# Optimization experiments

Measured on AMD Instinct MI355X. Metric: run time of the kernel, lower is better.

## Reference

```python
import jax, jax.numpy as jnp
import numpy as np


def silu(x):
    return x * jax.nn.sigmoid(x)


def setup_inputs() -> dict:
    key = jax.random.key(0)
    B, L, Din = 2, 512, 128
    E, K = 2, 4
    d = E * Din          # inner dim = 256
    N = d                # state size forced to hid_dim = expansion*input_dim
    R = d // 16          # dt low-rank = 16
    ks = jax.random.split(key, 12)
    s = 0.02
    rn = lambda k, sh: (jax.random.normal(k, sh, jnp.float32) * s)
    return {
        "x":      jax.random.normal(ks[0], (B, L, Din), jnp.float32),
        "W_in":   rn(ks[1], (Din, d)),  "b_in":  jnp.zeros((d,), jnp.float32),
        "W_res":  rn(ks[2], (Din, d)),  "b_res": jnp.zeros((d,), jnp.float32),
        "conv_w": rn(ks[3], (d, d, K)), "conv_b": jnp.zeros((d,), jnp.float32),
        "W_xdt":  rn(ks[4], (d, R)),
        "W_dt":   rn(ks[5], (R, d)),
        "b_dt":   jnp.full((d,), -4.6, jnp.float32),  # softplus -> dt ~ 0.01
        "W_B":    rn(ks[6], (d, N)),
        "W_C":    rn(ks[7], (d, N)),
        "A_log":  jnp.log(jnp.broadcast_to(jnp.arange(1, N + 1, dtype=jnp.float32), (d, N))),
        "D":      jnp.ones((d,), jnp.float32),
        "W_out":  rn(ks[8], (d, Din)), "b_out": jnp.zeros((Din,), jnp.float32),
    }


def reference(x, W_in, b_in, W_res, b_res, conv_w, conv_b,
              W_xdt, W_dt, b_dt, W_B, W_C, A_log, D, W_out, b_out):
    k = conv_w.shape[-1]
    # input projections
    xi = x @ W_in + b_in               # [B,L,d]
    x_res = silu(x @ W_res + b_res)    # [B,L,d] gate branch
    # causal full (groups=1) conv1d: padding k-1, truncated to length L
    c = jax.lax.conv_general_dilated(
        xi.transpose(0, 2, 1), conv_w, window_strides=(1,),
        padding=[(k - 1, 0)], dimension_numbers=("NCH", "OIH", "NCH"))
    u = silu((c + conv_b[None, :, None]).transpose(0, 2, 1))  # [B,L,d]
    # S6 selective scan
    delta = jax.nn.softplus((u @ W_xdt) @ W_dt + b_dt)  # [B,L,d]
    Bm = u @ W_B                                        # [B,L,N]
    Cm = u @ W_C                                        # [B,L,N]
    A = -jnp.exp(A_log)                                 # [d,N]

    def step(h, xs):
        u_t, d_t, B_t, C_t = xs                         # [B,d],[B,d],[B,N],[B,N]
        dA = jnp.exp(d_t[:, :, None] * A)               # [B,d,N]
        h = dA * h + (d_t * u_t)[:, :, None] * B_t[:, None, :]
        y = jnp.einsum("bdn,bn->bd", h, C_t)
        return h, y

    h0 = jnp.zeros((x.shape[0], A.shape[0], A.shape[1]), xi.dtype)
    xs = (u.transpose(1, 0, 2), delta.transpose(1, 0, 2),
          Bm.transpose(1, 0, 2), Cm.transpose(1, 0, 2))
    _, ys = jax.lax.scan(step, h0, xs)                  # ys: [L,B,d]
    y = ys.transpose(1, 0, 2) + u * D                   # skip connection D*u
    # residual gate + output projection (norm disabled)
    return (y + x_res) @ W_out + b_out
```

## Files before the change

kernel.cpp:

```cpp
#include <hip/hip_runtime.h>
#include <hip/hip_bf16.h>

#define kB   2
#define kL   512
#define kBL  1024
#define kDin 128
#define kD   256
#define kN   256
#define kR   16
#define kK   4
#define kS   8
#define kT   64

__device__ __forceinline__ float silu_f(float v) { return v / (1.f + __expf(-v)); }
__device__ __forceinline__ float softplus_f(float z) {
    return (z > 20.f) ? z : log1pf(__expf(z));
}
__device__ __forceinline__ float4 f4fma(float s, float4 w, float4 a) {
    a.x += s * w.x; a.y += s * w.y; a.z += s * w.z; a.w += s * w.w; return a;
}

__global__ void __launch_bounds__(256) pre_kernel(
        const float* __restrict__ x, const float* __restrict__ W_in,
        const float* __restrict__ b_in, const float* __restrict__ W_res,
        const float* __restrict__ b_res, const float* __restrict__ conv_w,
        float* __restrict__ wT, float* __restrict__ xi, float* __restrict__ xres) {
    __shared__ float tile[32][33];
    __shared__ float xs[2][kDin];
    __shared__ float red[128][9];
    int bid = blockIdx.x, tid = threadIdx.x;
    if (bid < 256) {
        int c0 = (bid & 31) * 32, r0 = (bid >> 5) * 32;
        int tx = tid & 31, ty = tid >> 5;
        #pragma unroll
        for (int j = 0; j < 32; j += 8)
            tile[ty + j][tx] = conv_w[(r0 + ty + j) * 1024 + c0 + tx];
        __syncthreads();
        #pragma unroll
        for (int j = 0; j < 32; j += 8)
            wT[(c0 + ty + j) * 256 + r0 + tx] = tile[tx][ty + j];
        return;
    }
    int bt0 = (bid - 256) * 2;
    xs[tid >> 7][tid & 127] = x[bt0 * kDin + tid];
    __syncthreads();
    int q = tid & 63, m = (tid >> 6) & 1, ks = tid >> 7;
    const float* W = m ? W_res : W_in;
    float4 a0 = {0,0,0,0}, a1 = {0,0,0,0};
    int i0 = ks * 64;
    #pragma unroll 4
    for (int i = i0; i < i0 + 64; i++) {
        float4 w = ((const float4*)(W + i * kD))[q];
        a0 = f4fma(xs[0][i], w, a0);
        a1 = f4fma(xs[1][i], w, a1);
    }
    if (ks) {
        float* rr = red[tid - 128];
        rr[0] = a0.x; rr[1] = a0.y; rr[2] = a0.z; rr[3] = a0.w;
        rr[4] = a1.x; rr[5] = a1.y; rr[6] = a1.z; rr[7] = a1.w;
    }
    __syncthreads();
    if (!ks) {
        const float* rr = red[tid];
        a0.x += rr[0]; a0.y += rr[1]; a0.z += rr[2]; a0.w += rr[3];
        a1.x += rr[4]; a1.y += rr[5]; a1.z += rr[6]; a1.w += rr[7];
        float4 bv = ((const float4*)(m ? b_res : b_in))[q];
        a0.x += bv.x; a0.y += bv.y; a0.z += bv.z; a0.w += bv.w;
        a1.x += bv.x; a1.y += bv.y; a1.z += bv.z; a1.w += bv.w;
        if (m) {
            float4 s0 = {silu_f(a0.x), silu_f(a0.y), silu_f(a0.z), silu_f(a0.w)};
            float4 s1 = {silu_f(a1.x), silu_f(a1.y), silu_f(a1.z), silu_f(a1.w)};
            ((float4*)(xres + (bt0 + 0) * kD))[q] = s0;
            ((float4*)(xres + (bt0 + 1) * kD))[q] = s1;
        } else {
            ((float4*)(xi + (bt0 + 0) * kD))[q] = a0;
            ((float4*)(xi + (bt0 + 1) * kD))[q] = a1;
        }
    }
}

__global__ void __launch_bounds__(512) conv_fwd(
        const float* __restrict__ xi, const float* __restrict__ wT,
        const float* __restrict__ conv_b, float* __restrict__ u) {
    __shared__ float xs[7][kD];
    __shared__ float red[7][64][17];
    int bid = blockIdx.x, tid = threadIdx.x;
    int b = bid >> 7, t0 = (bid & 127) * 4;
    for (int idx = tid; idx < 7 * kD; idx += 512) {
        int j = idx >> 8, i = idx & 255;
        int t = t0 - 3 + j;
        xs[j][i] = (t >= 0) ? xi[(b * kL + t) * kD + i] : 0.f;
    }
    __syncthreads();
    int q = tid & 63, ks = tid >> 6;
    float4 a[4] = {{0,0,0,0},{0,0,0,0},{0,0,0,0},{0,0,0,0}};
    int ik0 = ks * 128;
    #pragma unroll 4
    for (int ik = ik0; ik < ik0 + 128; ik++) {
        float4 w = ((const float4*)(wT + ik * kD))[q];
        int ii = ik >> 2, k = ik & 3;
        #pragma unroll
        for (int r = 0; r < 4; r++) a[r] = f4fma(xs[k + r][ii], w, a[r]);
    }
    if (ks) {
        float* rr = red[ks - 1][q];
        #pragma unroll
        for (int r = 0; r < 4; r++) {
            rr[4*r+0] = a[r].x; rr[4*r+1] = a[r].y;
            rr[4*r+2] = a[r].z; rr[4*r+3] = a[r].w;
        }
    }
    __syncthreads();
    if (!ks) {
        #pragma unroll
        for (int p = 0; p < 7; p++) {
            const float* rr = red[p][q];
            #pragma unroll
            for (int r = 0; r < 4; r++) {
                a[r].x += rr[4*r+0]; a[r].y += rr[4*r+1];
                a[r].z += rr[4*r+2]; a[r].w += rr[4*r+3];
            }
        }
        float4 cb = ((const float4*)conv_b)[q];
        #pragma unroll
        for (int r = 0; r < 4; r++) {
            float4 v = {silu_f(a[r].x + cb.x), silu_f(a[r].y + cb.y),
                        silu_f(a[r].z + cb.z), silu_f(a[r].w + cb.w)};
            ((float4*)(u + (b * kL + t0 + r) * kD))[q] = v;
        }
    }
}

__global__ void __launch_bounds__(256) proj_bcd(
        const float* __restrict__ u, const float* __restrict__ W_xdt,
        const float* __restrict__ W_dt, const float* __restrict__ b_dt,
        const float* __restrict__ W_B, const float* __restrict__ W_C,
        float* __restrict__ delta, float* __restrict__ Bm, float* __restrict__ Cm) {
    __shared__ float us[2][kD];
    __shared__ float tpart[128];
    __shared__ float ts[2][kR];
    __shared__ float red[128][9];
    int bt0 = blockIdx.x * 2, tid = threadIdx.x;
    us[0][tid] = u[(bt0 + 0) * kD + tid];
    us[1][tid] = u[(bt0 + 1) * kD + tid];
    __syncthreads();
    if (tid < 128) {
        int r = tid >> 6, j = (tid >> 2) & 15, kq = tid & 3;
        float acc = 0.f;
        #pragma unroll 4
        for (int i = kq * 64; i < kq * 64 + 64; i++)
            acc += us[r][i] * W_xdt[i * kR + j];
        tpart[tid] = acc;
    }
    __syncthreads();
    if (tid < 32) {
        int r = tid >> 4, j = tid & 15;
        int base = r * 64 + j * 4;
        ts[r][j] = tpart[base] + tpart[base+1] + tpart[base+2] + tpart[base+3];
    }
    __syncthreads();
    int q = tid & 63, m = (tid >> 6) & 1, ks = tid >> 7;
    const float* W = m ? W_C : W_B;
    float4 a0 = {0,0,0,0}, a1 = {0,0,0,0};
    int i0 = ks * 128;
    #pragma unroll 4
    for (int i = i0; i < i0 + 128; i++) {
        float4 w = ((const float4*)(W + i * kN))[q];
        a0 = f4fma(us[0][i], w, a0);
        a1 = f4fma(us[1][i], w, a1);
    }
    if (ks) {
        float* rr = red[tid - 128];
        rr[0] = a0.x; rr[1] = a0.y; rr[2] = a0.z; rr[3] = a0.w;
        rr[4] = a1.x; rr[5] = a1.y; rr[6] = a1.z; rr[7] = a1.w;
    }
    __syncthreads();
    if (!ks) {
        const float* rr = red[tid];
        a0.x += rr[0]; a0.y += rr[1]; a0.z += rr[2]; a0.w += rr[3];
        a1.x += rr[4]; a1.y += rr[5]; a1.z += rr[6]; a1.w += rr[7];
        float* O = m ? Cm : Bm;
        ((float4*)(O + (bt0 + 0) * kN))[q] = a0;
        ((float4*)(O + (bt0 + 1) * kN))[q] = a1;
    }
    if (tid < 64) {
        float4 d0 = {0,0,0,0}, d1 = {0,0,0,0};
        #pragma unroll
        for (int j = 0; j < kR; j++) {
            float4 w = ((const float4*)(W_dt + j * kD))[tid];
            d0 = f4fma(ts[0][j], w, d0);
            d1 = f4fma(ts[1][j], w, d1);
        }
        float4 bd = ((const float4*)b_dt)[tid];
        float4 o0 = {softplus_f(d0.x + bd.x), softplus_f(d0.y + bd.y),
                     softplus_f(d0.z + bd.z), softplus_f(d0.w + bd.w)};
        float4 o1 = {softplus_f(d1.x + bd.x), softplus_f(d1.y + bd.y),
                     softplus_f(d1.z + bd.z), softplus_f(d1.w + bd.w)};
        ((float4*)(delta + (bt0 + 0) * kD))[tid] = o0;
        ((float4*)(delta + (bt0 + 1) * kD))[tid] = o1;
    }
}

__global__ void __launch_bounds__(1024, 4) scan_fused(
        const float* __restrict__ delta, const float* __restrict__ u,
        const float* __restrict__ Bm, const float* __restrict__ Cm,
        const float* __restrict__ A_log, float* __restrict__ ys) {
    __shared__ float4 hp4[2][kS][64];
    __shared__ float dt_s[16][kT];
    __shared__ float du_s[16][kT];
    __shared__ float dsumS[2][kS];
    int w = threadIdx.x >> 6, lane = threadIdx.x & 63;
    int s = w & 7, dd = w >> 3;
    int b = blockIdx.x >> 7, dp = blockIdx.x & 127;
    int d = dp * 2 + dd;

    float4 al = ((const float4*)(A_log + d * kN))[lane];
    float A0 = -__expf(al.x), A1 = -__expf(al.y);
    float A2 = -__expf(al.z), A3 = -__expf(al.w);

    int gtu = (b * kL + s * kT + lane) * kD + d;
    float my_dt = delta[gtu];
    float my_du = my_dt * u[gtu];

    float dsum = my_dt;
    #pragma unroll
    for (int off = 32; off; off >>= 1) dsum += __shfl_xor(dsum, off, 64);

    dt_s[w][lane] = my_dt;
    du_s[w][lane] = my_du;

    const float4* Bp = (const float4*)(Bm + (b * kL + s * kT) * kN) + lane;
    const float4* Cp = (const float4*)(Cm + (b * kL + s * kT) * kN) + lane;
    __syncthreads();

    float h0 = 0, h1 = 0, h2 = 0, h3 = 0;
    float my_y = 0.f;
    int i1 = lane & 1, i2 = lane & 2;

    auto scan_seg_y = [&]() {
        for (int c = 0; c < kT; c += 4) {
            float4 dt4 = *(const float4*)&dt_s[w][c];
            float4 du4 = *(const float4*)&du_s[w][c];
            float4 Bb[4], Cc[4];
            #pragma unroll
            for (int j = 0; j < 4; j++) {
                Bb[j] = Bp[(c + j) * (kN / 4)];
                Cc[j] = Cp[(c + j) * (kN / 4)];
            }
            float dts[4] = {dt4.x, dt4.y, dt4.z, dt4.w};
            float dus[4] = {du4.x, du4.y, du4.z, du4.w};
            float e[4][4];
            #pragma unroll
            for (int j = 0; j < 4; j++) {
                e[j][0] = __expf(dts[j] * A0);
                e[j][1] = __expf(dts[j] * A1);
                e[j][2] = __expf(dts[j] * A2);
                e[j][3] = __expf(dts[j] * A3);
            }
            float yp[4];
            #pragma unroll
            for (int j = 0; j < 4; j++) {
                h0 = e[j][0] * h0 + dus[j] * Bb[j].x;
                h1 = e[j][1] * h1 + dus[j] * Bb[j].y;
                h2 = e[j][2] * h2 + dus[j] * Bb[j].z;
                h3 = e[j][3] * h3 + dus[j] * Bb[j].w;
                yp[j] = h0 * Cc[j].x + h1 * Cc[j].y + h2 * Cc[j].z + h3 * Cc[j].w;
            }
            float u0 = i1 ? yp[0] : yp[1];
            float u1 = i1 ? yp[2] : yp[3];
            float v0 = __shfl_xor(u0, 1, 64);
            float v1 = __shfl_xor(u1, 1, 64);
            if (i1) { yp[0] = v0; yp[2] = v1; } else { yp[1] = v0; yp[3] = v1; }
            u0 = i2 ? yp[0] : yp[2];
            u1 = i2 ? yp[1] : yp[3];
            v0 = __shfl_xor(u0, 2, 64);
            v1 = __shfl_xor(u1, 2, 64);
            if (i2) { yp[0] = v0; yp[1] = v1; } else { yp[2] = v0; yp[3] = v1; }
            float acc = (yp[0] + yp[1]) + (yp[2] + yp[3]);
            acc += __shfl_xor(acc, 4, 64);
            acc += __shfl_xor(acc, 8, 64);
            acc += __shfl_xor(acc, 16, 64);
            acc += __shfl_xor(acc, 32, 64);
            my_y = ((lane >> 2) == (c >> 2)) ? acc : my_y;
        }
    };
    auto scan_seg = [&]() {
        #pragma unroll 4
        for (int c = 0; c < kT; c += 4) {
            float4 dt4 = *(const float4*)&dt_s[w][c];
            float4 du4 = *(const float4*)&du_s[w][c];
            float4 Bb[4];
            #pragma unroll
            for (int j = 0; j < 4; j++) Bb[j] = Bp[(c + j) * (kN / 4)];
            float dts[4] = {dt4.x, dt4.y, dt4.z, dt4.w};
            float dus[4] = {du4.x, du4.y, du4.z, du4.w};
            float e[4][4];
            #pragma unroll
            for (int j = 0; j < 4; j++) {
                e[j][0] = __expf(dts[j] * A0);
                e[j][1] = __expf(dts[j] * A1);
                e[j][2] = __expf(dts[j] * A2);
                e[j][3] = __expf(dts[j] * A3);
            }
            #pragma unroll
            for (int j = 0; j < 4; j++) {
                h0 = e[j][0] * h0 + dus[j] * Bb[j].x;
                h1 = e[j][1] * h1 + dus[j] * Bb[j].y;
                h2 = e[j][2] * h2 + dus[j] * Bb[j].z;
                h3 = e[j][3] * h3 + dus[j] * Bb[j].w;
            }
        }
    };

    if (s == 0) {
        scan_seg_y();
        hp4[dd][0][lane] = make_float4(h0, h1, h2, h3);
    } else if (s < 7) {
        scan_seg();
        hp4[dd][s][lane] = make_float4(h0, h1, h2, h3);
    }
    if (lane == 0) dsumS[dd][s] = dsum;
    __syncthreads();

    if (s > 0) {
        h0 = h1 = h2 = h3 = 0;
        float P = 0.f;
        for (int j = s - 1; j >= 0; j--) {
            float4 hv = hp4[dd][j][lane];
            h0 += __expf(A0 * P) * hv.x;
            h1 += __expf(A1 * P) * hv.y;
            h2 += __expf(A2 * P) * hv.z;
            h3 += __expf(A3 * P) * hv.w;
            P += dsumS[dd][j];
        }
        scan_seg_y();
    }
    ys[(b * kL + s * kT + lane) * kD + d] = my_y;
}

__global__ void __launch_bounds__(256) out_proj(
        const float* __restrict__ ys, const float* __restrict__ u,
        const float* __restrict__ Dv, const float* __restrict__ xres,
        const float* __restrict__ W_out, const float* __restrict__ b_out,
        float* __restrict__ out) {
    __shared__ float vs[2][kD];
    __shared__ float red[224][9];
    int bt0 = blockIdx.x * 2, tid = threadIdx.x;
    for (int idx = tid; idx < 512; idx += 256) {
        int r = idx >> 8, i = idx & 255;
        int g = (bt0 + r) * kD + i;
        vs[r][i] = ys[g] + u[g] * Dv[i] + xres[g];
    }
    __syncthreads();
    int q = tid & 31, ks = tid >> 5;
    float4 a0 = {0,0,0,0}, a1 = {0,0,0,0};
    int i0 = ks * 32;
    #pragma unroll 4
    for (int i = i0; i < i0 + 32; i++) {
        float4 w = ((const float4*)(W_out + i * kDin))[q];
        a0 = f4fma(vs[0][i], w, a0);
        a1 = f4fma(vs[1][i], w, a1);
    }
    if (ks) {
        float* rr = red[tid - 32];
        rr[0] = a0.x; rr[1] = a0.y; rr[2] = a0.z; rr[3] = a0.w;
        rr[4] = a1.x; rr[5] = a1.y; rr[6] = a1.z; rr[7] = a1.w;
    }
    __syncthreads();
    if (!ks) {
        #pragma unroll
        for (int p = 0; p < 7; p++) {
            const float* rr = red[p * 32 + tid];
            a0.x += rr[0]; a0.y += rr[1]; a0.z += rr[2]; a0.w += rr[3];
            a1.x += rr[4]; a1.y += rr[5]; a1.z += rr[6]; a1.w += rr[7];
        }
        float4 bv = ((const float4*)b_out)[q];
        a0.x += bv.x; a0.y += bv.y; a0.z += bv.z; a0.w += bv.w;
        a1.x += bv.x; a1.y += bv.y; a1.z += bv.z; a1.w += bv.w;
        ((float4*)(out + (bt0 + 0) * kDin))[q] = a0;
        ((float4*)(out + (bt0 + 1) * kDin))[q] = a1;
    }
}

extern "C" void kernel_launch(void* const* d_in, const int* in_sizes, int n_in,
                              void* d_out, int out_size, void* d_ws, size_t ws_size,
                              hipStream_t stream) {
    const float* x      = (const float*)d_in[0];
    const float* W_in   = (const float*)d_in[1];
    const float* b_in   = (const float*)d_in[2];
    const float* W_res  = (const float*)d_in[3];
    const float* b_res  = (const float*)d_in[4];
    const float* conv_w = (const float*)d_in[5];
    const float* conv_b = (const float*)d_in[6];
    const float* W_xdt  = (const float*)d_in[7];
    const float* W_dt   = (const float*)d_in[8];
    const float* b_dt   = (const float*)d_in[9];
    const float* W_B    = (const float*)d_in[10];
    const float* W_C    = (const float*)d_in[11];
    const float* A_log  = (const float*)d_in[12];
    const float* Dv     = (const float*)d_in[13];
    const float* W_out  = (const float*)d_in[14];
    const float* b_out  = (const float*)d_in[15];

    float* ws    = (float*)d_ws;
    float* slot0 = ws;
    float* xres  = ws + 1 * 262144;
    float* slot2 = ws + 2 * 262144;
    float* u     = ws + 3 * 262144;
    float* yss   = ws + 4 * 262144;
    float* Cmat  = ws + 5 * 262144;

    float* xi    = slot0;
    float* delta = slot0;
    float* wT    = slot2;
    float* Bmat  = slot2;

    pre_kernel<<<768, 256, 0, stream>>>(x, W_in, b_in, W_res, b_res, conv_w,
                                        wT, xi, xres);
    conv_fwd<<<256, 512, 0, stream>>>(xi, wT, conv_b, u);
    proj_bcd<<<512, 256, 0, stream>>>(u, W_xdt, W_dt, b_dt, W_B, W_C,
                                      delta, Bmat, Cmat);
    scan_fused<<<kB * 128, 1024, 0, stream>>>(delta, u, Bmat, Cmat, A_log, yss);
    out_proj<<<512, 256, 0, stream>>>(yss, u, Dv, xres, W_out, b_out,
                                      (float*)d_out);
}
```

Measured before the change: 172.6 us.

## Fuse conv and B/C/delta projections; fold D-skip and gate into scan

Merges the conv kernel and the B/C/delta projection kernel into one kernel that keeps the four conv output rows in shared memory and projects them directly. This removes one launch and the global re-read of u. It also moves the D*u + x_res addition into the scan epilogue, so out_proj reads one tensor instead of three. The trade-off is more shared memory and a larger register footprint in the fused kernel, whose projection phase runs on only 256 blocks. The workspace layout is changed so delta and Bm no longer alias xi and wT.

```diff
diff --git a/kernel.cpp b/kernel.cpp
--- a/kernel.cpp
+++ b/kernel.cpp
@@ -79,11 +79,19 @@
     }
 }
 
-__global__ void __launch_bounds__(512) conv_fwd(
+__global__ void __launch_bounds__(512) conv_bcd(
         const float* __restrict__ xi, const float* __restrict__ wT,
-        const float* __restrict__ conv_b, float* __restrict__ u) {
+        const float* __restrict__ conv_b, const float* __restrict__ W_xdt,
+        const float* __restrict__ W_dt, const float* __restrict__ b_dt,
+        const float* __restrict__ W_B, const float* __restrict__ W_C,
+        float* __restrict__ u, float* __restrict__ delta,
+        float* __restrict__ Bm, float* __restrict__ Cm) {
     __shared__ float xs[7][kD];
+    __shared__ float us[4][kD];
     __shared__ float red[7][64][17];
+    __shared__ float red2[3][128][17];
+    __shared__ float tpart[256];
+    __shared__ float ts[4][kR];
     int bid = blockIdx.x, tid = threadIdx.x;
     int b = bid >> 7, t0 = (bid & 127) * 4;
     for (int idx = tid; idx < 7 * kD; idx += 512) {
@@ -92,59 +100,58 @@
         xs[j][i] = (t >= 0) ? xi[(b * kL + t) * kD + i] : 0.f;
     }
     __syncthreads();
-    int q = tid & 63, ks = tid >> 6;
-    float4 a[4] = {{0,0,0,0},{0,0,0,0},{0,0,0,0},{0,0,0,0}};
-    int ik0 = ks * 128;
+    int q = tid & 63, ks8 = tid >> 6;
+    {
+        float4 a[4] = {{0,0,0,0},{0,0,0,0},{0,0,0,0},{0,0,0,0}};
+        int ik0 = ks8 * 128;
+        #pragma unroll 4
+        for (int ik = ik0; ik < ik0 + 128; ik++) {
+            float4 w = ((const float4*)(wT + ik * kD))[q];
+            int ii = ik >> 2, k = ik & 3;
+            #pragma unroll
+            for (int r = 0; r < 4; r++) a[r] = f4fma(xs[k + r][ii], w, a[r]);
+        }
+        if (ks8) {
+            float* rr = red[ks8 - 1][q];
+            #pragma unroll
+            for (int r = 0; r < 4; r++) {
+                rr[4*r+0] = a[r].x; rr[4*r+1] = a[r].y;
+                rr[4*r+2] = a[r].z; rr[4*r+3] = a[r].w;
+            }
+        }
+        __syncthreads();
+        if (!ks8) {
+            #pragma unroll
+            for (int p = 0; p < 7; p++) {
+                const float* rr = red[p][q];
+                #pragma unroll
+                for (int r = 0; r < 4; r++) {
+                    a[r].x += rr[4*r+0]; a[r].y += rr[4*r+1];
+                    a[r].z += rr[4*r+2]; a[r].w += rr[4*r+3];
+                }
+            }
+            float4 cb = ((const float4*)conv_b)[q];
+            #pragma unroll
+            for (int r = 0; r < 4; r++) {
+                float4 v = {silu_f(a[r].x + cb.x), silu_f(a[r].y + cb.y),
+                            silu_f(a[r].z + cb.z), silu_f(a[r].w + cb.w)};
+                *(float4*)&us[r][4 * q] = v;
+                ((float4*)(u + (b * kL + t0 + r) * kD))[q] = v;
+            }
+        }
+    }
+    __syncthreads();
+    int m = (tid >> 6) & 1, ks4 = tid >> 7;
+    const float* W = m ? W_C : W_B;
+    float4 acc4[4] = {{0,0,0,0},{0,0,0,0},{0,0,0,0},{0,0,0,0}};
+    int i0 = ks4 * 64;
     #pragma unroll 4
-    for (int ik = ik0; ik < ik0 + 128; ik++) {
-        float4 w = ((const float4*)(wT + ik * kD))[q];
-        int ii = ik >> 2, k = ik & 3;
-        #pragma unroll
-        for (int r = 0; r < 4; r++) a[r] = f4fma(xs[k + r][ii], w, a[r]);
-    }
-    if (ks) {
-        float* rr = red[ks - 1][q];
-        #pragma unroll
-        for (int r = 0; r < 4; r++) {
-            rr[4*r+0] = a[r].x; rr[4*r+1] = a[r].y;
-            rr[4*r+2] = a[r].z; rr[4*r+3] = a[r].w;
-        }
-    }
-    __syncthreads();
-    if (!ks) {
-        #pragma unroll
-        for (int p = 0; p < 7; p++) {
-            const float* rr = red[p][q];
-            #pragma unroll
-            for (int r = 0; r < 4; r++) {
-                a[r].x += rr[4*r+0]; a[r].y += rr[4*r+1];
-                a[r].z += rr[4*r+2]; a[r].w += rr[4*r+3];
-            }
-        }
-        float4 cb = ((const float4*)conv_b)[q];
-        #pragma unroll
-        for (int r = 0; r < 4; r++) {
-            float4 v = {silu_f(a[r].x + cb.x), silu_f(a[r].y + cb.y),
-                        silu_f(a[r].z + cb.z), silu_f(a[r].w + cb.w)};
-            ((float4*)(u + (b * kL + t0 + r) * kD))[q] = v;
-        }
-    }
-}
-
-__global__ void __launch_bounds__(256) proj_bcd(
-        const float* __restrict__ u, const float* __restrict__ W_xdt,
-        const float* __restrict__ W_dt, const float* __restrict__ b_dt,
-        const float* __restrict__ W_B, const float* __restrict__ W_C,
-        float* __restrict__ delta, float* __restrict__ Bm, float* __restrict__ Cm) {
-    __shared__ float us[2][kD];
-    __shared__ float tpart[128];
-    __shared__ float ts[2][kR];
-    __shared__ float red[128][9];
-    int bt0 = blockIdx.x * 2, tid = threadIdx.x;
-    us[0][tid] = u[(bt0 + 0) * kD + tid];
-    us[1][tid] = u[(bt0 + 1) * kD + tid];
-    __syncthreads();
-    if (tid < 128) {
+    for (int i = i0; i < i0 + 64; i++) {
+        float4 w = ((const float4*)(W + i * kN))[q];
+        #pragma unroll
+        for (int r = 0; r < 4; r++) acc4[r] = f4fma(us[r][i], w, acc4[r]);
+    }
+    if (tid < 256) {
         int r = tid >> 6, j = (tid >> 2) & 15, kq = tid & 3;
         float acc = 0.f;
         #pragma unroll 4
@@ -152,59 +159,56 @@
             acc += us[r][i] * W_xdt[i * kR + j];
         tpart[tid] = acc;
     }
-    __syncthreads();
-    if (tid < 32) {
+    if (ks4) {
+        float* rr = red2[ks4 - 1][tid & 127];
+        #pragma unroll
+        for (int r = 0; r < 4; r++) {
+            rr[4*r+0] = acc4[r].x; rr[4*r+1] = acc4[r].y;
+            rr[4*r+2] = acc4[r].z; rr[4*r+3] = acc4[r].w;
+        }
+    }
+    __syncthreads();
+    if (!ks4) {
+        #pragma unroll
+        for (int p = 0; p < 3; p++) {
+            const float* rr = red2[p][tid];
+            #pragma unroll
+            for (int r = 0; r < 4; r++) {
+                acc4[r].x += rr[4*r+0]; acc4[r].y += rr[4*r+1];
+                acc4[r].z += rr[4*r+2]; acc4[r].w += rr[4*r+3];
+            }
+        }
+        float* O = m ? Cm : Bm;
+        #pragma unroll
+        for (int r = 0; r < 4; r++)
+            ((float4*)(O + (b * kL + t0 + r) * kN))[q] = acc4[r];
+    }
+    if (tid < 64) {
         int r = tid >> 4, j = tid & 15;
         int base = r * 64 + j * 4;
         ts[r][j] = tpart[base] + tpart[base+1] + tpart[base+2] + tpart[base+3];
     }
     __syncthreads();
-    int q = tid & 63, m = (tid >> 6) & 1, ks = tid >> 7;
-    const float* W = m ? W_C : W_B;
-    float4 a0 = {0,0,0,0}, a1 = {0,0,0,0};
-    int i0 = ks * 128;
-    #pragma unroll 4
-    for (int i = i0; i < i0 + 128; i++) {
-        float4 w = ((const float4*)(W + i * kN))[q];
-        a0 = f4fma(us[0][i], w, a0);
-        a1 = f4fma(us[1][i], w, a1);
-    }
-    if (ks) {
-        float* rr = red[tid - 128];
-        rr[0] = a0.x; rr[1] = a0.y; rr[2] = a0.z; rr[3] = a0.w;
-        rr[4] = a1.x; rr[5] = a1.y; rr[6] = a1.z; rr[7] = a1.w;
-    }
-    __syncthreads();
-    if (!ks) {
-        const float* rr = red[tid];
-        a0.x += rr[0]; a0.y += rr[1]; a0.z += rr[2]; a0.w += rr[3];
-        a1.x += rr[4]; a1.y += rr[5]; a1.z += rr[6]; a1.w += rr[7];
-        float* O = m ? Cm : Bm;
-        ((float4*)(O + (bt0 + 0) * kN))[q] = a0;
-        ((float4*)(O + (bt0 + 1) * kN))[q] = a1;
-    }
-    if (tid < 64) {
-        float4 d0 = {0,0,0,0}, d1 = {0,0,0,0};
+    if (tid < 256) {
+        int r = tid >> 6;
+        float4 dacc = {0,0,0,0};
         #pragma unroll
         for (int j = 0; j < kR; j++) {
-            float4 w = ((const float4*)(W_dt + j * kD))[tid];
-            d0 = f4fma(ts[0][j], w, d0);
-            d1 = f4fma(ts[1][j], w, d1);
-        }
-        float4 bd = ((const float4*)b_dt)[tid];
-        float4 o0 = {softplus_f(d0.x + bd.x), softplus_f(d0.y + bd.y),
-                     softplus_f(d0.z + bd.z), softplus_f(d0.w + bd.w)};
-        float4 o1 = {softplus_f(d1.x + bd.x), softplus_f(d1.y + bd.y),
-                     softplus_f(d1.z + bd.z), softplus_f(d1.w + bd.w)};
-        ((float4*)(delta + (bt0 + 0) * kD))[tid] = o0;
-        ((float4*)(delta + (bt0 + 1) * kD))[tid] = o1;
+            float4 w = ((const float4*)(W_dt + j * kD))[q];
+            dacc = f4fma(ts[r][j], w, dacc);
+        }
+        float4 bd = ((const float4*)b_dt)[q];
+        float4 o0 = {softplus_f(dacc.x + bd.x), softplus_f(dacc.y + bd.y),
+                     softplus_f(dacc.z + bd.z), softplus_f(dacc.w + bd.w)};
+        ((float4*)(delta + (b * kL + t0 + r) * kD))[q] = o0;
     }
 }
 
 __global__ void __launch_bounds__(1024, 4) scan_fused(
         const float* __restrict__ delta, const float* __restrict__ u,
         const float* __restrict__ Bm, const float* __restrict__ Cm,
-        const float* __restrict__ A_log, float* __restrict__ ys) {
+        const float* __restrict__ A_log, const float* __restrict__ Dv,
+        const float* __restrict__ xres, float* __restrict__ yfull) {
     __shared__ float4 hp4[2][kS][64];
     __shared__ float dt_s[16][kT];
     __shared__ float du_s[16][kT];
@@ -220,7 +224,9 @@
 
     int gtu = (b * kL + s * kT + lane) * kD + d;
     float my_dt = delta[gtu];
-    float my_du = my_dt * u[gtu];
+    float my_u  = u[gtu];
+    float my_du = my_dt * my_u;
+    float fold  = Dv[d] * my_u + xres[gtu];
 
     float dsum = my_dt;
     #pragma unroll
@@ -335,21 +341,18 @@
         }
         scan_seg_y();
     }
-    ys[(b * kL + s * kT + lane) * kD + d] = my_y;
+    yfull[gtu] = my_y + fold;
 }
 
 __global__ void __launch_bounds__(256) out_proj(
-        const float* __restrict__ ys, const float* __restrict__ u,
-        const float* __restrict__ Dv, const float* __restrict__ xres,
-        const float* __restrict__ W_out, const float* __restrict__ b_out,
-        float* __restrict__ out) {
+        const float* __restrict__ yfull, const float* __restrict__ W_out,
+        const float* __restrict__ b_out, float* __restrict__ out) {
     __shared__ float vs[2][kD];
     __shared__ float red[224][9];
     int bt0 = blockIdx.x * 2, tid = threadIdx.x;
     for (int idx = tid; idx < 512; idx += 256) {
         int r = idx >> 8, i = idx & 255;
-        int g = (bt0 + r) * kD + i;
-        vs[r][i] = ys[g] + u[g] * Dv[i] + xres[g];
+        vs[r][i] = yfull[(bt0 + r) * kD + i];
     }
     __syncthreads();
     int q = tid & 31, ks = tid >> 5;
@@ -403,24 +406,20 @@
     const float* b_out  = (const float*)d_in[15];
 
     float* ws    = (float*)d_ws;
-    float* slot0 = ws;
+    float* xi    = ws + 0 * 262144;
     float* xres  = ws + 1 * 262144;
-    float* slot2 = ws + 2 * 262144;
+    float* wT    = ws + 2 * 262144;
     float* u     = ws + 3 * 262144;
-    float* yss   = ws + 4 * 262144;
+    float* yfull = ws + 4 * 262144;
     float* Cmat  = ws + 5 * 262144;
-
-    float* xi    = slot0;
-    float* delta = slot0;
-    float* wT    = slot2;
-    float* Bmat  = slot2;
+    float* delta = ws + 6 * 262144;
+    float* Bmat  = ws + 7 * 262144;
 
     pre_kernel<<<768, 256, 0, stream>>>(x, W_in, b_in, W_res, b_res, conv_w,
                                         wT, xi, xres);
-    conv_fwd<<<256, 512, 0, stream>>>(xi, wT, conv_b, u);
-    proj_bcd<<<512, 256, 0, stream>>>(u, W_xdt, W_dt, b_dt, W_B, W_C,
-                                      delta, Bmat, Cmat);
-    scan_fused<<<kB * 128, 1024, 0, stream>>>(delta, u, Bmat, Cmat, A_log, yss);
-    out_proj<<<512, 256, 0, stream>>>(yss, u, Dv, xres, W_out, b_out,
-                                      (float*)d_out);
-}
+    conv_bcd<<<256, 512, 0, stream>>>(xi, wT, conv_b, W_xdt, W_dt, b_dt,
+                                      W_B, W_C, u, delta, Bmat, Cmat);
+    scan_fused<<<kB * 128, 1024, 0, stream>>>(delta, u, Bmat, Cmat, A_log,
+                                              Dv, xres, yfull);
+    out_proj<<<512, 256, 0, stream>>>(yfull, W_out, b_out, (float*)d_out);
+}
```

After: 163.0 us. 5.6% less time.
